# Optimization experiments

Measured on AMD Instinct MI355X. Metric: run time of the kernel, lower is better.

The kernel has to match this reference:

```python
import jax, jax.numpy as jnp
import numpy as np

B, S, I, H, O = 4096, 512, 1, 16, 1


def setup_inputs() -> dict:
    key = jax.random.key(0)
    ks = jax.random.split(key, 7)
    bound = 1.0 / np.sqrt(H)
    return {
        "x": jax.random.normal(ks[0], (B, S, I), dtype=jnp.float32),
        "W_ih": jax.random.uniform(ks[1], (H, I), minval=-bound, maxval=bound, dtype=jnp.float32),
        "W_hh": jax.random.uniform(ks[2], (H, H), minval=-bound, maxval=bound, dtype=jnp.float32),
        "b_ih": jax.random.uniform(ks[3], (H,), minval=-bound, maxval=bound, dtype=jnp.float32),
        "b_hh": jax.random.uniform(ks[4], (H,), minval=-bound, maxval=bound, dtype=jnp.float32),
        "W_fc": jax.random.uniform(ks[5], (O, H), minval=-bound, maxval=bound, dtype=jnp.float32),
        "b_fc": jax.random.uniform(ks[6], (O,), minval=-bound, maxval=bound, dtype=jnp.float32),
    }


def reference(x, W_ih, W_hh, b_ih, b_hh, W_fc, b_fc):
    # Vanilla RNN (tanh): h_t = tanh(x_t W_ih^T + b_ih + h_{t-1} W_hh^T + b_hh)
    # Precompute input projections for all timesteps in one GEMM: [B,S,H]
    x_proj = jnp.einsum('bsi,hi->bsh', x, W_ih) + b_ih + b_hh

    def step(h, xp_t):  # h: [B,H], xp_t: [B,H]
        h_new = jnp.tanh(xp_t + h @ W_hh.T)
        return h_new, None

    h0 = jnp.zeros((x.shape[0], W_hh.shape[0]), dtype=x.dtype)
    h_last, _ = jax.lax.scan(step, h0, jnp.swapaxes(x_proj, 0, 1))  # scan over S
    # out[:, -1, :] -> final linear
    return h_last @ W_fc.T + b_fc
```

## Files before the change

### kernel.cpp

```cpp
#include <hip/hip_runtime.h>


#define S2LE 2.8853900817779268f

#define ROTI(v, N) __builtin_amdgcn_mov_dpp((v), 0x120 + (N), 0xF, 0xF, 0)
#define ROTF(v, N) __int_as_float(__builtin_amdgcn_mov_dpp(__float_as_int(v), 0x120 + (N), 0xF, 0xF, 0))

__global__ __launch_bounds__(64) void rnn_kernel(
    const float* __restrict__ x,
    const float* __restrict__ W_ih,
    const float* __restrict__ W_hh,
    const float* __restrict__ b_ih,
    const float* __restrict__ b_hh,
    const float* __restrict__ W_fc,
    const float* __restrict__ b_fc,
    float* __restrict__ out)
{
    const int li = (int)(threadIdx.x & 15u);
    const int b  = (int)((blockIdx.x * 64u + threadIdx.x) >> 4);

    const float* __restrict__ row = W_hh + li * 16;

    float sw = 0.0f;
#pragma unroll
    for (int j = 0; j < 16; ++j) sw += row[j];

    float wg[16];
    wg[0] = -2.0f * S2LE * row[li];
#define LW(N) { int s_ = ROTI(li, N); wg[N] = -2.0f * S2LE * row[s_]; }
    LW(1) LW(2) LW(3) LW(4) LW(5) LW(6) LW(7) LW(8)
    LW(9) LW(10) LW(11) LW(12) LW(13) LW(14) LW(15)
#undef LW

    const float wih  = W_ih[li] * S2LE;
    const float bias = (b_ih[li] + b_hh[li] + sw) * S2LE;
    const float wfc  = W_fc[li];
    const float bfc  = b_fc[0];

    const float4* __restrict__ xv = (const float4*)(x + (size_t)b * 512);

    float g = 0.5f;
    float4 xc = xv[0];

#define STEP(XP) do { \
    float y0 = (XP); \
    y0 = fmaf(g,           wg[0],  y0); \
    y0 = fmaf(ROTF(g, 1),  wg[1],  y0); \
    y0 = fmaf(ROTF(g, 2),  wg[2],  y0); \
    y0 = fmaf(ROTF(g, 3),  wg[3],  y0); \
    float y1 =  ROTF(g, 4) * wg[4]; \
    y1 = fmaf(ROTF(g, 5),  wg[5],  y1); \
    y1 = fmaf(ROTF(g, 6),  wg[6],  y1); \
    y1 = fmaf(ROTF(g, 7),  wg[7],  y1); \
    float y2 =  ROTF(g, 8) * wg[8]; \
    y2 = fmaf(ROTF(g, 9),  wg[9],  y2); \
    y2 = fmaf(ROTF(g, 10), wg[10], y2); \
    y2 = fmaf(ROTF(g, 11), wg[11], y2); \
    float y3 =  ROTF(g, 12) * wg[12]; \
    y3 = fmaf(ROTF(g, 13), wg[13], y3); \
    y3 = fmaf(ROTF(g, 14), wg[14], y3); \
    y3 = fmaf(ROTF(g, 15), wg[15], y3); \
    float s_ = (y0 + y1) + (y2 + y3); \
    float e_ = __builtin_amdgcn_exp2f(s_); \
    g = __builtin_amdgcn_rcpf(e_ + 1.0f); \
} while (0)

#pragma unroll 1
    for (int c = 0; c < 128; ++c) {
        float4 xn = xv[(c + 1) & 127];
        float xp0 = fmaf(xc.x, wih, bias);
        float xp1 = fmaf(xc.y, wih, bias);
        float xp2 = fmaf(xc.z, wih, bias);
        float xp3 = fmaf(xc.w, wih, bias);
        STEP(xp0);
        STEP(xp1);
        STEP(xp2);
        STEP(xp3);
        xc = xn;
    }
#undef STEP

    float p = fmaf(-2.0f * wfc, g, wfc);
    p += ROTF(p, 8);
    p += ROTF(p, 4);
    p += ROTF(p, 2);
    p += ROTF(p, 1);
    if (li == 0) out[b] = p + bfc;
}

extern "C" void kernel_launch(void* const* d_in, const int* in_sizes, int n_in,
                              void* d_out, int out_size, void* d_ws, size_t ws_size,
                              hipStream_t stream) {
    const float* x    = (const float*)d_in[0];
    const float* W_ih = (const float*)d_in[1];
    const float* W_hh = (const float*)d_in[2];
    const float* b_ih = (const float*)d_in[3];
    const float* b_hh = (const float*)d_in[4];
    const float* W_fc = (const float*)d_in[5];
    const float* b_fc = (const float*)d_in[6];
    float* out = (float*)d_out;

    rnn_kernel<<<1024, 64, 0, stream>>>(x, W_ih, W_hh, b_ih, b_hh, W_fc, b_fc, out);
}
```

Before: 106.6 us.

## Use packed fp16 dot2 for recurrent matvec and deepen x prefetch

```diff
diff --git a/kernel.cpp b/kernel.cpp
--- a/kernel.cpp
+++ b/kernel.cpp
@@ -3,8 +3,12 @@
 
 #define S2LE 2.8853900817779268f
 
+typedef __fp16 half2_ __attribute__((ext_vector_type(2)));
+typedef float float4_ __attribute__((ext_vector_type(4)));
+
 #define ROTI(v, N) __builtin_amdgcn_mov_dpp((v), 0x120 + (N), 0xF, 0xF, 0)
 #define ROTF(v, N) __int_as_float(__builtin_amdgcn_mov_dpp(__float_as_int(v), 0x120 + (N), 0xF, 0xF, 0))
+#define ROTP(v, N) __builtin_bit_cast(half2_, __builtin_amdgcn_mov_dpp(__builtin_bit_cast(int, (v)), 0x120 + (N), 0xF, 0xF, 0))
 
 __global__ __launch_bounds__(64) void rnn_kernel(
     const float* __restrict__ x,
@@ -25,58 +29,67 @@
 #pragma unroll
     for (int j = 0; j < 16; ++j) sw += row[j];
 
-    float wg[16];
-    wg[0] = -2.0f * S2LE * row[li];
-#define LW(N) { int s_ = ROTI(li, N); wg[N] = -2.0f * S2LE * row[s_]; }
-    LW(1) LW(2) LW(3) LW(4) LW(5) LW(6) LW(7) LW(8)
-    LW(9) LW(10) LW(11) LW(12) LW(13) LW(14) LW(15)
+    const float wsc = -2.0f * S2LE;
+
+    half2_ w2[8];
+    {
+        const int r1i = ROTI(li, 1);
+        w2[0][0] = (__fp16)(wsc * row[li]);
+        w2[0][1] = (__fp16)(wsc * row[r1i]);
+#define LW(K, N) { int s0_ = ROTI(li, N); int s1_ = ROTI(r1i, N); \
+        w2[K][0] = (__fp16)(wsc * row[s0_]); \
+        w2[K][1] = (__fp16)(wsc * row[s1_]); }
+        LW(1, 2) LW(2, 4) LW(3, 6) LW(4, 8) LW(5, 10) LW(6, 12) LW(7, 14)
 #undef LW
+    }
 
     const float wih  = W_ih[li] * S2LE;
     const float bias = (b_ih[li] + b_hh[li] + sw) * S2LE;
     const float wfc  = W_fc[li];
     const float bfc  = b_fc[0];
 
-    const float4* __restrict__ xv = (const float4*)(x + (size_t)b * 512);
+    const float4_* __restrict__ xv = (const float4_*)(x + (size_t)b * 512);
 
     float g = 0.5f;
-    float4 xc = xv[0];
+    float4_ xc = xv[0];
+    float4_ xn = xv[1];
 
 #define STEP(XP) do { \
-    float y0 = (XP); \
-    y0 = fmaf(g,           wg[0],  y0); \
-    y0 = fmaf(ROTF(g, 1),  wg[1],  y0); \
-    y0 = fmaf(ROTF(g, 2),  wg[2],  y0); \
-    y0 = fmaf(ROTF(g, 3),  wg[3],  y0); \
-    float y1 =  ROTF(g, 4) * wg[4]; \
-    y1 = fmaf(ROTF(g, 5),  wg[5],  y1); \
-    y1 = fmaf(ROTF(g, 6),  wg[6],  y1); \
-    y1 = fmaf(ROTF(g, 7),  wg[7],  y1); \
-    float y2 =  ROTF(g, 8) * wg[8]; \
-    y2 = fmaf(ROTF(g, 9),  wg[9],  y2); \
-    y2 = fmaf(ROTF(g, 10), wg[10], y2); \
-    y2 = fmaf(ROTF(g, 11), wg[11], y2); \
-    float y3 =  ROTF(g, 12) * wg[12]; \
-    y3 = fmaf(ROTF(g, 13), wg[13], y3); \
-    y3 = fmaf(ROTF(g, 14), wg[14], y3); \
-    y3 = fmaf(ROTF(g, 15), wg[15], y3); \
-    float s_ = (y0 + y1) + (y2 + y3); \
+    float r1_ = ROTF(g, 1); \
+    half2_ pk0 = __builtin_amdgcn_cvt_pkrtz(g, r1_); \
+    half2_ p2_  = ROTP(pk0, 2); \
+    half2_ p4_  = ROTP(pk0, 4); \
+    half2_ p6_  = ROTP(pk0, 6); \
+    half2_ p8_  = ROTP(pk0, 8); \
+    half2_ p10_ = ROTP(pk0, 10); \
+    half2_ p12_ = ROTP(pk0, 12); \
+    half2_ p14_ = ROTP(pk0, 14); \
+    float c0_ = __builtin_amdgcn_fdot2(pk0,  w2[0], (XP), false); \
+    c0_ = __builtin_amdgcn_fdot2(p2_,  w2[1], c0_, false); \
+    float c1_ = __builtin_amdgcn_fdot2(p4_,  w2[2], 0.0f, false); \
+    c1_ = __builtin_amdgcn_fdot2(p6_,  w2[3], c1_, false); \
+    float c2_ = __builtin_amdgcn_fdot2(p8_,  w2[4], 0.0f, false); \
+    c2_ = __builtin_amdgcn_fdot2(p10_, w2[5], c2_, false); \
+    float c3_ = __builtin_amdgcn_fdot2(p12_, w2[6], 0.0f, false); \
+    c3_ = __builtin_amdgcn_fdot2(p14_, w2[7], c3_, false); \
+    float s_ = (c0_ + c1_) + (c2_ + c3_); \
     float e_ = __builtin_amdgcn_exp2f(s_); \
     g = __builtin_amdgcn_rcpf(e_ + 1.0f); \
 } while (0)
 
 #pragma unroll 1
     for (int c = 0; c < 128; ++c) {
-        float4 xn = xv[(c + 1) & 127];
-        float xp0 = fmaf(xc.x, wih, bias);
-        float xp1 = fmaf(xc.y, wih, bias);
-        float xp2 = fmaf(xc.z, wih, bias);
-        float xp3 = fmaf(xc.w, wih, bias);
+        float4_ xf = xv[(c + 2) & 127];
+        float xp0 = fmaf(xc[0], wih, bias);
+        float xp1 = fmaf(xc[1], wih, bias);
+        float xp2 = fmaf(xc[2], wih, bias);
+        float xp3 = fmaf(xc[3], wih, bias);
         STEP(xp0);
         STEP(xp1);
         STEP(xp2);
         STEP(xp3);
         xc = xn;
+        xn = xf;
     }
 #undef STEP
 
```

Result: no change. 104.7 us (-1.8%).
